# Kernel tuning notes

Measured on AMD Instinct MI355X. Metric: run time of the kernel, lower is better.

The kernel has to match this reference:

```python
import jax, jax.numpy as jnp
import numpy as np

B, T, HID = 2, 2048, 1536
H, HKV, D = 12, 2, 128
EPS = 1e-6
NEG = -1e9


def setup_inputs() -> dict:
    key = jax.random.key(0)
    ks = jax.random.split(key, 8)
    # rotary embeddings built from real angles (cos/sin of position*inv_freq)
    inv_freq = 1.0 / (10000.0 ** (jnp.arange(0, D, 2, dtype=jnp.float32) / D))  # [D/2]
    pos = jnp.arange(T, dtype=jnp.float32)
    ang = pos[:, None] * inv_freq[None, :]                       # [T, D/2]
    emb = jnp.concatenate([ang, ang], axis=-1)                   # [T, D]
    cos = jnp.broadcast_to(jnp.cos(emb)[None], (B, T, D))
    sin = jnp.broadcast_to(jnp.sin(emb)[None], (B, T, D))
    # additive causal mask [1,1,T,T]
    causal = jnp.tril(jnp.ones((T, T), dtype=bool))
    attention_mask = jnp.where(causal, 0.0, NEG).astype(jnp.float32)[None, None]
    s = 0.02
    return {
        "hidden_states": jax.random.normal(ks[0], (B, T, HID), jnp.float32),
        "cos": cos,
        "sin": sin,
        "attention_mask": attention_mask,
        "q_w": jax.random.normal(ks[1], (H * D, HID), jnp.float32) * s,
        "k_w": jax.random.normal(ks[2], (HKV * D, HID), jnp.float32) * s,
        "v_w": jax.random.normal(ks[3], (HKV * D, HID), jnp.float32) * s,
        "o_w": jax.random.normal(ks[4], (HID, H * D), jnp.float32) * s,
        "q_norm_w": jnp.ones((D,), jnp.float32),
        "k_norm_w": jnp.ones((D,), jnp.float32),
    }


def _rms_norm(x, w):
    # per-head RMSNorm over last dim (head_dim), computed in fp32
    xf = x.astype(jnp.float32)
    var = jnp.mean(xf * xf, axis=-1, keepdims=True)
    return (w * (xf * jax.lax.rsqrt(var + EPS))).astype(x.dtype)


def _rotate_half(x):
    x1, x2 = jnp.split(x, 2, axis=-1)
    return jnp.concatenate([-x2, x1], axis=-1)


def reference(hidden_states, cos, sin, attention_mask, q_w, k_w, v_w, o_w, q_norm_w, k_norm_w):
    b, t, _ = hidden_states.shape
    n_rep = H // HKV
    scale = D ** -0.5

    # projections -> [B, n_heads, T, D]
    q = (hidden_states @ q_w.T).reshape(b, t, H, D)
    k = (hidden_states @ k_w.T).reshape(b, t, HKV, D)
    v = (hidden_states @ v_w.T).reshape(b, t, HKV, D).transpose(0, 2, 1, 3)

    # per-head QK RMSNorm, then to [B, H, T, D]
    q = _rms_norm(q, q_norm_w).transpose(0, 2, 1, 3)
    k = _rms_norm(k, k_norm_w).transpose(0, 2, 1, 3)

    # RoPE (cos/sin broadcast over head axis)
    c = cos[:, None, :, :]
    s = sin[:, None, :, :]
    q = q * c + _rotate_half(q) * s
    k = k * c + _rotate_half(k) * s

    # GQA repeat_kv: [B, HKV, T, D] -> [B, H, T, D]
    k = jnp.repeat(k, n_rep, axis=1)
    v = jnp.repeat(v, n_rep, axis=1)

    attn = jnp.einsum('bhqd,bhkd->bhqk', q, k) * scale + attention_mask
    attn = jax.nn.softmax(attn.astype(jnp.float32), axis=-1).astype(q.dtype)
    out = jnp.einsum('bhqk,bhkd->bhqd', attn, v)
    out = out.transpose(0, 2, 1, 3).reshape(b, t, H * D)
    return out @ o_w.T
```

## Files before the change

### kernel.cpp

```cpp
#include <hip/hip_runtime.h>
#include <hip/hip_bf16.h>


#define B_   2
#define T_   2048
#define HID_ 1536
#define H_   12
#define HKV_ 2
#define D_   128
#define GQ_  (H_ / HKV_)
#define NQKV_ 2048
#define SCALE_ 0.08838834764831845f

typedef unsigned short u16;
typedef __attribute__((ext_vector_type(4))) float f32x4;
typedef __attribute__((ext_vector_type(8))) short bf16x8;
typedef __attribute__((ext_vector_type(4))) unsigned short u16x4;
typedef __attribute__((ext_vector_type(8))) unsigned short u16x8;

__device__ __forceinline__ u16 f2b(float f) {
  union { __hip_bfloat16 h; u16 u; } cv;
  cv.h = __float2bfloat16(f);
  return cv.u;
}
__device__ __forceinline__ float b2f(u16 u) {
  union { float f; unsigned i; } cv;
  cv.i = ((unsigned)u) << 16;
  return cv.f;
}

__device__ __forceinline__ void glds16(const u16* g, u16* l) {
  __builtin_amdgcn_global_load_lds((const __attribute__((address_space(1))) void*)g,
                                   (__attribute__((address_space(3))) void*)l, 16, 0, 0);
}

__global__ __launch_bounds__(256) void cvt_f32_bf16(const float* __restrict__ src,
                                                    u16* __restrict__ dst, int n4) {
  int i = blockIdx.x * 256 + threadIdx.x;
  const int stride = gridDim.x * 256;
  for (; i < n4; i += stride) {
    const float4 v = reinterpret_cast<const float4*>(src)[i];
    u16x4 o = {f2b(v.x), f2b(v.y), f2b(v.z), f2b(v.w)};
    reinterpret_cast<u16x4*>(dst)[i] = o;
  }
}

#define NQ4_ 589824
#define NK4_ 98304
__global__ __launch_bounds__(256) void cvt_wqkv(const float* __restrict__ q_w,
                                                const float* __restrict__ k_w,
                                                const float* __restrict__ v_w,
                                                u16* __restrict__ qkvw) {
  int i = blockIdx.x * 256 + threadIdx.x;
  const int stride = gridDim.x * 256;
  const int total = NQ4_ + 2 * NK4_;
  for (; i < total; i += stride) {
    float4 v;
    if (i < NQ4_) v = reinterpret_cast<const float4*>(q_w)[i];
    else if (i < NQ4_ + NK4_) v = reinterpret_cast<const float4*>(k_w)[i - NQ4_];
    else v = reinterpret_cast<const float4*>(v_w)[i - NQ4_ - NK4_];
    u16x4 o = {f2b(v.x), f2b(v.y), f2b(v.z), f2b(v.w)};
    reinterpret_cast<u16x4*>(qkvw)[i] = o;
  }
}

__global__ __launch_bounds__(256) void gemm_bt(const u16* __restrict__ A,
                                               const u16* __restrict__ W,
                                               float* __restrict__ C,
                                               int M, int N, int K) {
  __shared__ __align__(16) u16 As[128 * 64];
  __shared__ __align__(16) u16 Ws[128 * 64];
  const int tid  = threadIdx.x;
  const int lane = tid & 63;
  const int wid  = tid >> 6;
  const int wr = wid >> 1, wc = wid & 1;
  const int l15 = lane & 15, kg = lane >> 4;
  const int rowBase = blockIdx.y * 128;
  const int colBase = blockIdx.x * 128;

  const int srow = lane >> 3;
  const int scol = (lane & 7) << 3;
  const u16* Ab = A + (size_t)(rowBase + wid * 32 + srow) * K + scol;
  const u16* Wb = W + (size_t)(colBase + wid * 32 + srow) * K + scol;

  const f32x4 zero4 = {0.f, 0.f, 0.f, 0.f};
  f32x4 acc[4][4];
#pragma unroll
  for (int m = 0; m < 4; ++m)
#pragma unroll
    for (int n = 0; n < 4; ++n) acc[m][n] = zero4;

  for (int k0 = 0; k0 < K; k0 += 64) {
    __syncthreads();
#pragma unroll
    for (int c = 0; c < 4; ++c) {
      glds16(Ab + (size_t)(c * 8) * K + k0, &As[(wid * 4 + c) * 512]);
      glds16(Wb + (size_t)(c * 8) * K + k0, &Ws[(wid * 4 + c) * 512]);
    }
    __syncthreads();
    bf16x8 a[4][2], b[4][2];
#pragma unroll
    for (int m = 0; m < 4; ++m)
#pragma unroll
      for (int ks = 0; ks < 2; ++ks)
        a[m][ks] = *reinterpret_cast<const bf16x8*>(
            &As[(wr * 64 + m * 16 + l15) * 64 + ks * 32 + kg * 8]);
#pragma unroll
    for (int n = 0; n < 4; ++n)
#pragma unroll
      for (int ks = 0; ks < 2; ++ks)
        b[n][ks] = *reinterpret_cast<const bf16x8*>(
            &Ws[(wc * 64 + n * 16 + l15) * 64 + ks * 32 + kg * 8]);
#pragma unroll
    for (int m = 0; m < 4; ++m)
#pragma unroll
      for (int n = 0; n < 4; ++n)
#pragma unroll
        for (int ks = 0; ks < 2; ++ks)
          acc[m][n] = __builtin_amdgcn_mfma_f32_16x16x32_bf16(a[m][ks], b[n][ks],
                                                              acc[m][n], 0, 0, 0);
  }
#pragma unroll
  for (int m = 0; m < 4; ++m) {
    const int row0 = rowBase + wr * 64 + m * 16 + kg * 4;
#pragma unroll
    for (int n = 0; n < 4; ++n) {
      const int col = colBase + wc * 64 + n * 16 + l15;
#pragma unroll
      for (int r = 0; r < 4; ++r) C[(size_t)(row0 + r) * N + col] = acc[m][n][r];
    }
  }
}

__global__ __launch_bounds__(256) void gemm_qkv(
    const u16* __restrict__ A, const u16* __restrict__ W,
    const float* __restrict__ cosb, const float* __restrict__ sinb,
    const float* __restrict__ q_nw, const float* __restrict__ k_nw,
    u16* __restrict__ q_b, u16* __restrict__ k_b, u16* __restrict__ vt_b) {
  __shared__ __align__(16) u16 smem[128 * 137];
  u16* As = smem;
  u16* Ws = smem + 8192;
  const int tid  = threadIdx.x;
  const int lane = tid & 63;
  const int wid  = tid >> 6;
  const int wr = wid >> 1, wc = wid & 1;
  const int l15 = lane & 15, kg = lane >> 4;
  const int rowBase = blockIdx.y * 128;
  const int colBase = blockIdx.x * 128;
  const int K = HID_;

  const int srow = lane >> 3;
  const int scol = (lane & 7) << 3;
  const u16* Ab = A + (size_t)(rowBase + wid * 32 + srow) * K + scol;
  const u16* Wb = W + (size_t)(colBase + wid * 32 + srow) * K + scol;

  const f32x4 zero4 = {0.f, 0.f, 0.f, 0.f};
  f32x4 acc[4][4];
#pragma unroll
  for (int m = 0; m < 4; ++m)
#pragma unroll
    for (int n = 0; n < 4; ++n) acc[m][n] = zero4;

  for (int k0 = 0; k0 < K; k0 += 64) {
    __syncthreads();
#pragma unroll
    for (int c = 0; c < 4; ++c) {
      glds16(Ab + (size_t)(c * 8) * K + k0, &As[(wid * 4 + c) * 512]);
      glds16(Wb + (size_t)(c * 8) * K + k0, &Ws[(wid * 4 + c) * 512]);
    }
    __syncthreads();
    bf16x8 a[4][2], b[4][2];
#pragma unroll
    for (int m = 0; m < 4; ++m)
#pragma unroll
      for (int ks = 0; ks < 2; ++ks)
        a[m][ks] = *reinterpret_cast<const bf16x8*>(
            &As[(wr * 64 + m * 16 + l15) * 64 + ks * 32 + kg * 8]);
#pragma unroll
    for (int n = 0; n < 4; ++n)
#pragma unroll
      for (int ks = 0; ks < 2; ++ks)
        b[n][ks] = *reinterpret_cast<const bf16x8*>(
            &Ws[(wc * 64 + n * 16 + l15) * 64 + ks * 32 + kg * 8]);
#pragma unroll
    for (int m = 0; m < 4; ++m)
#pragma unroll
      for (int n = 0; n < 4; ++n)
#pragma unroll
        for (int ks = 0; ks < 2; ++ks)
          acc[m][n] = __builtin_amdgcn_mfma_f32_16x16x32_bf16(a[m][ks], b[n][ks],
                                                              acc[m][n], 0, 0, 0);
  }

  __syncthreads();
#pragma unroll
  for (int m = 0; m < 4; ++m)
#pragma unroll
    for (int n = 0; n < 4; ++n)
#pragma unroll
      for (int r = 0; r < 4; ++r)
        smem[(wr * 64 + m * 16 + kg * 4 + r) * 137 + wc * 64 + n * 16 + l15] =
            f2b(acc[m][n][r]);
  __syncthreads();

  const int ct = blockIdx.x;
  const int b = rowBase >> 11;
  if (ct < 14) {
    const float* nw = (ct < 12) ? q_nw : k_nw;
    const float nwl = nw[lane], nwh = nw[lane + 64];
    const float sc = (ct < 12) ? SCALE_ : 1.0f;
    u16* dstbase = (ct < 12) ? (q_b + (size_t)(b * H_ + ct) * T_ * D_)
                             : (k_b + (size_t)(b * HKV_ + (ct - 12)) * T_ * D_);
    for (int i = 0; i < 32; ++i) {
      const int row = wid * 32 + i;
      const int tok = rowBase + row;
      const int t = tok & (T_ - 1);
      const float x1 = b2f(smem[row * 137 + lane]);
      const float x2 = b2f(smem[row * 137 + lane + 64]);
      float ss = x1 * x1 + x2 * x2;
#pragma unroll
      for (int msk = 32; msk >= 1; msk >>= 1) ss += __shfl_xor(ss, msk);
      const float rinv = rsqrtf(ss * (1.0f / D_) + 1e-6f);
      const float c1 = cosb[(size_t)tok * D_ + lane];
      const float c2 = cosb[(size_t)tok * D_ + lane + 64];
      const float s1 = sinb[(size_t)tok * D_ + lane];
      const float s2 = sinb[(size_t)tok * D_ + lane + 64];
      const float n1 = x1 * rinv * nwl, n2 = x2 * rinv * nwh;
      u16* dst = dstbase + (size_t)t * D_;
      dst[lane] = f2b((n1 * c1 - n2 * s1) * sc);
      dst[lane + 64] = f2b((n2 * c2 + n1 * s2) * sc);
    }
  } else {
    const int hv = ct - 14;
    const int tp = (lane & 32) | (((lane >> 2) & 3) << 3) | (((lane >> 4) & 1) << 2) |
                   (lane & 3);
    u16* vb = vt_b + (size_t)(b * HKV_ + hv) * D_ * T_;
    const int tb = rowBase & (T_ - 1);
    for (int it = 0; it < 64; ++it) {
      const int d = wid * 32 + (it >> 1), half = it & 1;
      const float x = b2f(smem[(half * 64 + lane) * 137 + d]);
      vb[(size_t)d * T_ + tb + half * 64 + tp] = f2b(x);
    }
  }
}

__constant__ int QT_ARR[40] = {15,15,15,15,14,14,11,11,11,10, 7, 7, 3,
                               14,14,13,13,13,13,12,12,10,10, 9, 9, 6, 6,
                               12,12, 9, 8, 8, 8, 5, 5, 2,
                                4, 4, 1, 0};
__constant__ int C_ARR[40]  = { 0, 1, 2, 3, 0, 1, 0, 1, 2, 0, 0, 1,-1,
                                2, 3, 0, 1, 2, 3, 0, 1, 1, 2, 0, 1, 0, 1,
                                2, 3, 2, 0, 1, 2, 0, 1,-1,
                                0, 1,-1,-1};
__device__ __forceinline__ int nc_of(int qt) { return (qt < 8) ? 2 : ((qt < 12) ? 3 : 4); }
__device__ __forceinline__ int mlbase_of(int qt) {
  return (qt < 8) ? 2 * (qt - 4) : ((qt < 12) ? 8 + 3 * (qt - 8) : 20 + 4 * (qt - 12));
}
__device__ __forceinline__ int pbase_of(int qt) {
  return (qt < 8) ? (qt - 4) : ((qt < 12) ? 4 + 2 * (qt - 8) : 12 + 3 * (qt - 12));
}

__global__ __launch_bounds__(256) void attn_kernel(const u16* __restrict__ q_b,
                                                   const u16* __restrict__ k_b,
                                                   const u16* __restrict__ vt_b,
                                                   u16* __restrict__ aout,
                                                   u16* __restrict__ po0,
                                                   float2* __restrict__ ml) {
  __shared__ __align__(16) u16 Ks[2][64 * 128];
  __shared__ __align__(16) u16 Vs[2][128 * 64];
  const int id = blockIdx.x;
  const int item = id / 24;
  const int bh = id - item * 24;
  const int qt = QT_ARR[item];
  const int c = C_ARR[item];
  int kt0, ktend;
  bool partial;
  if (c < 0) {
    kt0 = 0; ktend = 2 * qt + 1; partial = false;
  } else {
    const int nt = 2 * qt + 2;
    const int nc = nc_of(qt);
    const int base = nt / nc, rem = nt - base * nc;
    kt0 = c * base + (c < rem ? c : rem);
    ktend = kt0 + base + (c < rem ? 1 : 0) - 1;
    partial = true;
  }
  const int b = bh / H_, h = bh - b * H_;
  const int kvh = h / GQ_;
  const int tid = threadIdx.x;
  const int w = tid >> 6, lane = tid & 63;
  const int l15 = lane & 15, kg = lane >> 4;
  const int qbase = qt * 128;

  const u16* Kb = k_b + (size_t)(b * HKV_ + kvh) * T_ * D_;
  const u16* Vb = vt_b + (size_t)(b * HKV_ + kvh) * D_ * T_;

  bf16x8 qf[2][4];
#pragma unroll
  for (int qb = 0; qb < 2; ++qb) {
    const u16* qrow =
        q_b + ((size_t)(b * H_ + h) * T_ + qbase + w * 32 + qb * 16 + l15) * D_;
#pragma unroll
    for (int s4 = 0; s4 < 4; ++s4)
      qf[qb][s4] = *reinterpret_cast<const bf16x8*>(qrow + s4 * 32 + kg * 8);
  }

  int kK[4], vK[4];
#pragma unroll
  for (int cc = 0; cc < 4; ++cc) {
    const int ch = w * 4 + cc;
    const int kr = ch * 4 + (lane >> 4);
    kK[cc] = kr * D_ + (((lane & 15) << 3) ^ ((kr & 7) << 3));
    const int dr = ch * 8 + (lane >> 3);
    vK[cc] = dr * T_ + (((lane & 7) << 3) ^ ((dr & 7) << 3));
  }
  const int xorv = (l15 & 7) << 3;

  const f32x4 zero4 = {0.f, 0.f, 0.f, 0.f};
  f32x4 o[2][8];
#pragma unroll
  for (int qb = 0; qb < 2; ++qb)
#pragma unroll
    for (int n = 0; n < 8; ++n) o[qb][n] = zero4;
  float m[2] = {0.f, 0.f};
  float lsum[2] = {0.f, 0.f};

  {
    const size_t kb = (size_t)kt0 * 64;
#pragma unroll
    for (int cc = 0; cc < 4; ++cc) {
      glds16(Kb + kb * D_ + kK[cc], &Ks[0][(w * 4 + cc) * 512]);
      glds16(Vb + kb + vK[cc], &Vs[0][(w * 4 + cc) * 512]);
    }
  }
  int cur = 0;

  for (int kt = kt0; kt <= ktend; ++kt) {
    if (kt < ktend) {
      const size_t kb = (size_t)(kt + 1) * 64;
#pragma unroll
      for (int cc = 0; cc < 4; ++cc) {
        glds16(Kb + kb * D_ + kK[cc], &Ks[cur ^ 1][(w * 4 + cc) * 512]);
        glds16(Vb + kb + vK[cc], &Vs[cur ^ 1][(w * 4 + cc) * 512]);
      }
      asm volatile("s_waitcnt vmcnt(8)" ::: "memory");
    } else {
      asm volatile("s_waitcnt vmcnt(0)" ::: "memory");
    }
    __builtin_amdgcn_s_barrier();
    asm volatile("" ::: "memory");

    const u16* Kc = &Ks[cur][0];
    const u16* Vc = &Vs[cur][0];
    f32x4 sc[2][4];
#pragma unroll
    for (int qb = 0; qb < 2; ++qb)
#pragma unroll
      for (int n = 0; n < 4; ++n) sc[qb][n] = zero4;
    __builtin_amdgcn_s_setprio(1);
#pragma unroll
    for (int n = 0; n < 4; ++n)
#pragma unroll
      for (int s4 = 0; s4 < 4; ++s4) {
        const int koff = (n * 16 + l15) * 128 + ((s4 * 32 + kg * 8) ^ xorv);
        bf16x8 kf = *reinterpret_cast<const bf16x8*>(&Kc[koff]);
#pragma unroll
        for (int qb = 0; qb < 2; ++qb)
          sc[qb][n] = __builtin_amdgcn_mfma_f32_16x16x32_bf16(kf, qf[qb][s4],
                                                              sc[qb][n], 0, 0, 0);
      }
    __builtin_amdgcn_s_setprio(0);
    if (kt >= 2 * qt) {
#pragma unroll
      for (int qb = 0; qb < 2; ++qb) {
        const int qg = w * 32 + qb * 16 + l15;
        const int kbb = (kt - 2 * qt) * 64;
#pragma unroll
        for (int n = 0; n < 4; ++n)
#pragma unroll
          for (int r = 0; r < 4; ++r)
            if (kbb + n * 16 + kg * 4 + r > qg) sc[qb][n][r] = -3e38f;
      }
    }
    float pm[2];
#pragma unroll
    for (int qb = 0; qb < 2; ++qb) {
      float v = sc[qb][0][0];
#pragma unroll
      for (int n = 0; n < 4; ++n)
#pragma unroll
        for (int r = 0; r < 4; ++r) v = fmaxf(v, sc[qb][n][r]);
      v = fmaxf(v, __shfl_xor(v, 16));
      v = fmaxf(v, __shfl_xor(v, 32));
      pm[qb] = v;
    }
    if (__any((pm[0] > m[0] + 8.f) | (pm[1] > m[1] + 8.f))) {
#pragma unroll
      for (int qb = 0; qb < 2; ++qb) {
        const float mn = fmaxf(m[qb], pm[qb]);
        const float al = __expf(m[qb] - mn);
        m[qb] = mn;
        lsum[qb] *= al;
        float alT[4];
#pragma unroll
        for (int r = 0; r < 4; ++r)
          alT[r] = __shfl(al, (lane & 48) | (kg * 4 + r));
#pragma unroll
        for (int n = 0; n < 8; ++n)
#pragma unroll
          for (int r = 0; r < 4; ++r) o[qb][n][r] *= alT[r];
      }
    }
#pragma unroll
    for (int qb = 0; qb < 2; ++qb) {
      float rs = 0.f;
#pragma unroll
      for (int n = 0; n < 4; ++n)
#pragma unroll
        for (int r = 0; r < 4; ++r) {
          const float p = __expf(sc[qb][n][r] - m[qb]);
          sc[qb][n][r] = p;
          rs += p;
        }
      rs += __shfl_xor(rs, 16);
      rs += __shfl_xor(rs, 32);
      lsum[qb] += rs;
    }
    bf16x8 pf[2][2];
#pragma unroll
    for (int qb = 0; qb < 2; ++qb)
#pragma unroll
      for (int ks = 0; ks < 2; ++ks)
#pragma unroll
        for (int r = 0; r < 4; ++r) {
          pf[qb][ks][r] = (short)f2b(sc[qb][2 * ks][r]);
          pf[qb][ks][r + 4] = (short)f2b(sc[qb][2 * ks + 1][r]);
        }
    __builtin_amdgcn_s_setprio(1);
#pragma unroll
    for (int n = 0; n < 8; ++n)
#pragma unroll
      for (int ks = 0; ks < 2; ++ks) {
        const int voff = (n * 16 + l15) * 64 + ((ks * 32 + kg * 8) ^ xorv);
        bf16x8 vf = *reinterpret_cast<const bf16x8*>(&Vc[voff]);
#pragma unroll
        for (int qb = 0; qb < 2; ++qb)
          o[qb][n] = __builtin_amdgcn_mfma_f32_16x16x32_bf16(pf[qb][ks], vf,
                                                             o[qb][n], 0, 0, 0);
      }
    __builtin_amdgcn_s_setprio(0);
    __builtin_amdgcn_s_barrier();
    cur ^= 1;
  }

  if (!partial) {
    float invT[2][4];
#pragma unroll
    for (int qb = 0; qb < 2; ++qb) {
      const float inv = 1.0f / lsum[qb];
#pragma unroll
      for (int r = 0; r < 4; ++r)
        invT[qb][r] = __shfl(inv, (lane & 48) | (kg * 4 + r));
    }
#pragma unroll
    for (int qb = 0; qb < 2; ++qb) {
      const int t0 = qbase + w * 32 + qb * 16 + kg * 4;
#pragma unroll
      for (int n = 0; n < 8; ++n)
#pragma unroll
        for (int r = 0; r < 4; ++r)
          aout[(size_t)(b * T_ + t0 + r) * (H_ * D_) + h * D_ + n * 16 + l15] =
              f2b(o[qb][n][r] * invT[qb][r]);
    }
  } else {
    const int mlslot = bh * 36 + mlbase_of(qt) + c;
    if (kg == 0) {
#pragma unroll
      for (int qb = 0; qb < 2; ++qb) {
        float2 v;
        v.x = m[qb];
        v.y = lsum[qb];
        ml[(size_t)mlslot * 128 + w * 32 + qb * 16 + l15] = v;
      }
    }
    if (c == 0) {
#pragma unroll
      for (int qb = 0; qb < 2; ++qb) {
        const int t0 = qbase + w * 32 + qb * 16 + kg * 4;
#pragma unroll
        for (int n = 0; n < 8; ++n)
#pragma unroll
          for (int r = 0; r < 4; ++r)
            aout[(size_t)(b * T_ + t0 + r) * (H_ * D_) + h * D_ + n * 16 + l15] =
                f2b(o[qb][n][r]);
      }
    } else {
      const int pslot = bh * 24 + pbase_of(qt) + (c - 1);
#pragma unroll
      for (int qb = 0; qb < 2; ++qb) {
        const int row0 = w * 32 + qb * 16 + kg * 4;
#pragma unroll
        for (int n = 0; n < 8; ++n)
#pragma unroll
          for (int r = 0; r < 4; ++r)
            po0[((size_t)pslot * 128 + row0 + r) * 128 + n * 16 + l15] =
                f2b(o[qb][n][r]);
      }
    }
  }
}

__global__ __launch_bounds__(256) void combine_kernel(u16* __restrict__ aout,
                                                      const u16* __restrict__ po0,
                                                      const float2* __restrict__ ml) {
  const int qt = 4 + blockIdx.x;
  const int bh = blockIdx.y;
  const int nc = nc_of(qt);
  const int mlb = bh * 36 + mlbase_of(qt);
  const int pb = bh * 24 + pbase_of(qt);
  const int b = bh / H_, h = bh - b * H_;
  const int t0 = qt * 128;
  const int tid = threadIdx.x;
  const int row = tid >> 1;
  const int colc = (tid & 1) << 6;

  float ms[4], ls[4];
  float mm = -3e38f;
  for (int cc = 0; cc < nc; ++cc) {
    const float2 v = ml[(size_t)(mlb + cc) * 128 + row];
    ms[cc] = v.x; ls[cc] = v.y;
    mm = fmaxf(mm, v.x);
  }
  float lt = 0.f;
  float scl[4];
  for (int cc = 0; cc < nc; ++cc) {
    scl[cc] = __expf(ms[cc] - mm);
    lt += ls[cc] * scl[cc];
  }
  const float inv = 1.0f / lt;
  for (int cc = 0; cc < nc; ++cc) scl[cc] *= inv;

  u16* a = aout + (size_t)(b * T_ + t0 + row) * (H_ * D_) + h * D_ + colc;
#pragma unroll
  for (int j = 0; j < 8; ++j) {
    u16x8 v0 = *reinterpret_cast<const u16x8*>(a + j * 8);
    float acc[8];
#pragma unroll
    for (int e = 0; e < 8; ++e) acc[e] = b2f(v0[e]) * scl[0];
    for (int cc = 1; cc < nc; ++cc) {
      const u16* p = po0 + ((size_t)(pb + cc - 1) * 128 + row) * 128 + colc;
      u16x8 vc = *reinterpret_cast<const u16x8*>(p + j * 8);
#pragma unroll
      for (int e = 0; e < 8; ++e) acc[e] += b2f(vc[e]) * scl[cc];
    }
    u16x8 outv;
#pragma unroll
    for (int e = 0; e < 8; ++e) outv[e] = f2b(acc[e]);
    *reinterpret_cast<u16x8*>(a + j * 8) = outv;
  }
}

extern "C" void kernel_launch(void* const* d_in, const int* in_sizes, int n_in,
                              void* d_out, int out_size, void* d_ws, size_t ws_size,
                              hipStream_t stream) {
  const float* hidden = (const float*)d_in[0];
  const float* cosb   = (const float*)d_in[1];
  const float* sinb   = (const float*)d_in[2];
  const float* q_w  = (const float*)d_in[4];
  const float* k_w  = (const float*)d_in[5];
  const float* v_w  = (const float*)d_in[6];
  const float* o_w  = (const float*)d_in[7];
  const float* q_nw = (const float*)d_in[8];
  const float* k_nw = (const float*)d_in[9];
  float* out = (float*)d_out;

  char* ws = (char*)d_ws;
  const size_t MB = 1u << 20;
  u16*    hidden_b = (u16*)(ws);
  u16*    qkvw     = (u16*)(ws + 12 * MB);
  u16*    q_b      = (u16*)(ws + 18 * MB);
  u16*    k_b      = (u16*)(ws + 30 * MB);
  u16*    vt_b     = (u16*)(ws + 32 * MB);
  u16*    aout     = (u16*)(ws);
  u16*    owb      = (u16*)(ws + 12 * MB);
  float2* ml       = (float2*)(ws + 17 * MB);
  u16*    po0      = (u16*)d_out;

  const dim3 blk(256);
  const int M = B_ * T_;

  cvt_f32_bf16<<<2048, blk, 0, stream>>>(hidden, hidden_b, (B_ * T_ * HID_) / 4);
  cvt_wqkv<<<3072, blk, 0, stream>>>(q_w, k_w, v_w, qkvw);

  gemm_qkv<<<dim3(NQKV_ / 128, M / 128), blk, 0, stream>>>(
      hidden_b, qkvw, cosb, sinb, q_nw, k_nw, q_b, k_b, vt_b);

  cvt_f32_bf16<<<2048, blk, 0, stream>>>(o_w, owb, (H_ * D_ * HID_) / 4);

  attn_kernel<<<960, blk, 0, stream>>>(q_b, k_b, vt_b, aout, po0, ml);
  combine_kernel<<<dim3(12, B_ * H_), blk, 0, stream>>>(aout, po0, ml);

  gemm_bt<<<dim3(HID_ / 128, M / 128), blk, 0, stream>>>(aout, owb, out,
                                                         M, HID_, HID_);
}
```

Measured before the change: 202.1 us.

## Double-buffer LDS in both GEMMs and fuse input conversion kernels

Both GEMM kernels now use two LDS buffers, issuing the global-to-LDS loads for the next K tile before running the MFMAs on the current one. This cuts the per-iteration barriers from two to one and raises wave priority around the MFMA block. The hidden-state and QKV-weight fp32-to-bf16 conversions are merged into one launch to save a kernel dispatch. Doubling shared memory per block may lower occupancy, and the single waitcnt(0) barrier still serialises at every tile.

Result: faster. 189.8 us (-6.1%).

```diff
diff --git a/kernel.cpp b/kernel.cpp
--- a/kernel.cpp
+++ b/kernel.cpp
@@ -45,22 +45,33 @@
   }
 }
 
+#define NH4_ 1572864
 #define NQ4_ 589824
 #define NK4_ 98304
-__global__ __launch_bounds__(256) void cvt_wqkv(const float* __restrict__ q_w,
-                                                const float* __restrict__ k_w,
-                                                const float* __restrict__ v_w,
-                                                u16* __restrict__ qkvw) {
+__global__ __launch_bounds__(256) void cvt_inputs(const float* __restrict__ hidden,
+                                                  const float* __restrict__ q_w,
+                                                  const float* __restrict__ k_w,
+                                                  const float* __restrict__ v_w,
+                                                  u16* __restrict__ hidden_b,
+                                                  u16* __restrict__ qkvw) {
   int i = blockIdx.x * 256 + threadIdx.x;
   const int stride = gridDim.x * 256;
-  const int total = NQ4_ + 2 * NK4_;
+  const int total = NH4_ + NQ4_ + 2 * NK4_;
   for (; i < total; i += stride) {
     float4 v;
-    if (i < NQ4_) v = reinterpret_cast<const float4*>(q_w)[i];
-    else if (i < NQ4_ + NK4_) v = reinterpret_cast<const float4*>(k_w)[i - NQ4_];
-    else v = reinterpret_cast<const float4*>(v_w)[i - NQ4_ - NK4_];
+    u16x4* dst;
+    if (i < NH4_) {
+      v = reinterpret_cast<const float4*>(hidden)[i];
+      dst = reinterpret_cast<u16x4*>(hidden_b) + i;
+    } else {
+      const int j = i - NH4_;
+      if (j < NQ4_) v = reinterpret_cast<const float4*>(q_w)[j];
+      else if (j < NQ4_ + NK4_) v = reinterpret_cast<const float4*>(k_w)[j - NQ4_];
+      else v = reinterpret_cast<const float4*>(v_w)[j - NQ4_ - NK4_];
+      dst = reinterpret_cast<u16x4*>(qkvw) + j;
+    }
     u16x4 o = {f2b(v.x), f2b(v.y), f2b(v.z), f2b(v.w)};
-    reinterpret_cast<u16x4*>(qkvw)[i] = o;
+    *dst = o;
   }
 }
 
@@ -68,8 +79,8 @@
                                                const u16* __restrict__ W,
                                                float* __restrict__ C,
                                                int M, int N, int K) {
-  __shared__ __align__(16) u16 As[128 * 64];
-  __shared__ __align__(16) u16 Ws[128 * 64];
+  __shared__ __align__(16) u16 As[2][128 * 64];
+  __shared__ __align__(16) u16 Ws[2][128 * 64];
   const int tid  = threadIdx.x;
   const int lane = tid & 63;
   const int wid  = tid >> 6;
@@ -90,27 +101,40 @@
 #pragma unroll
     for (int n = 0; n < 4; ++n) acc[m][n] = zero4;
 
-  for (int k0 = 0; k0 < K; k0 += 64) {
-    __syncthreads();
-#pragma unroll
-    for (int c = 0; c < 4; ++c) {
-      glds16(Ab + (size_t)(c * 8) * K + k0, &As[(wid * 4 + c) * 512]);
-      glds16(Wb + (size_t)(c * 8) * K + k0, &Ws[(wid * 4 + c) * 512]);
-    }
-    __syncthreads();
+  const int nt = K >> 6;
+#pragma unroll
+  for (int c = 0; c < 4; ++c) {
+    glds16(Ab + (size_t)(c * 8) * K, &As[0][(wid * 4 + c) * 512]);
+    glds16(Wb + (size_t)(c * 8) * K, &Ws[0][(wid * 4 + c) * 512]);
+  }
+  asm volatile("s_waitcnt vmcnt(0)" ::: "memory");
+  __builtin_amdgcn_s_barrier();
+  asm volatile("" ::: "memory");
+  int cur = 0;
+
+  for (int t = 0; t < nt; ++t) {
+    if (t + 1 < nt) {
+      const int k0 = (t + 1) << 6;
+#pragma unroll
+      for (int c = 0; c < 4; ++c) {
+        glds16(Ab + (size_t)(c * 8) * K + k0, &As[cur ^ 1][(wid * 4 + c) * 512]);
+        glds16(Wb + (size_t)(c * 8) * K + k0, &Ws[cur ^ 1][(wid * 4 + c) * 512]);
+      }
+    }
     bf16x8 a[4][2], b[4][2];
 #pragma unroll
     for (int m = 0; m < 4; ++m)
 #pragma unroll
       for (int ks = 0; ks < 2; ++ks)
         a[m][ks] = *reinterpret_cast<const bf16x8*>(
-            &As[(wr * 64 + m * 16 + l15) * 64 + ks * 32 + kg * 8]);
+            &As[cur][(wr * 64 + m * 16 + l15) * 64 + ks * 32 + kg * 8]);
 #pragma unroll
     for (int n = 0; n < 4; ++n)
 #pragma unroll
       for (int ks = 0; ks < 2; ++ks)
         b[n][ks] = *reinterpret_cast<const bf16x8*>(
-            &Ws[(wc * 64 + n * 16 + l15) * 64 + ks * 32 + kg * 8]);
+            &Ws[cur][(wc * 64 + n * 16 + l15) * 64 + ks * 32 + kg * 8]);
+    __builtin_amdgcn_s_setprio(1);
 #pragma unroll
     for (int m = 0; m < 4; ++m)
 #pragma unroll
@@ -119,6 +143,13 @@
         for (int ks = 0; ks < 2; ++ks)
           acc[m][n] = __builtin_amdgcn_mfma_f32_16x16x32_bf16(a[m][ks], b[n][ks],
                                                               acc[m][n], 0, 0, 0);
+    __builtin_amdgcn_s_setprio(0);
+    if (t + 1 < nt) {
+      asm volatile("s_waitcnt vmcnt(0)" ::: "memory");
+      __builtin_amdgcn_s_barrier();
+      asm volatile("" ::: "memory");
+      cur ^= 1;
+    }
   }
 #pragma unroll
   for (int m = 0; m < 4; ++m) {
@@ -137,9 +168,7 @@
     const float* __restrict__ cosb, const float* __restrict__ sinb,
     const float* __restrict__ q_nw, const float* __restrict__ k_nw,
     u16* __restrict__ q_b, u16* __restrict__ k_b, u16* __restrict__ vt_b) {
-  __shared__ __align__(16) u16 smem[128 * 137];
-  u16* As = smem;
-  u16* Ws = smem + 8192;
+  __shared__ __align__(16) u16 smem[32768];
   const int tid  = threadIdx.x;
   const int lane = tid & 63;
   const int wid  = tid >> 6;
@@ -161,27 +190,42 @@
 #pragma unroll
     for (int n = 0; n < 4; ++n) acc[m][n] = zero4;
 
-  for (int k0 = 0; k0 < K; k0 += 64) {
-    __syncthreads();
-#pragma unroll
-    for (int c = 0; c < 4; ++c) {
-      glds16(Ab + (size_t)(c * 8) * K + k0, &As[(wid * 4 + c) * 512]);
-      glds16(Wb + (size_t)(c * 8) * K + k0, &Ws[(wid * 4 + c) * 512]);
-    }
-    __syncthreads();
+  const int nt = K >> 6;
+#pragma unroll
+  for (int c = 0; c < 4; ++c) {
+    glds16(Ab + (size_t)(c * 8) * K, &smem[(wid * 4 + c) * 512]);
+    glds16(Wb + (size_t)(c * 8) * K, &smem[8192 + (wid * 4 + c) * 512]);
+  }
+  asm volatile("s_waitcnt vmcnt(0)" ::: "memory");
+  __builtin_amdgcn_s_barrier();
+  asm volatile("" ::: "memory");
+  int cur = 0;
+
+  for (int t = 0; t < nt; ++t) {
+    if (t + 1 < nt) {
+      const int k0 = (t + 1) << 6;
+      const int ob = (cur ^ 1) * 16384;
+#pragma unroll
+      for (int c = 0; c < 4; ++c) {
+        glds16(Ab + (size_t)(c * 8) * K + k0, &smem[ob + (wid * 4 + c) * 512]);
+        glds16(Wb + (size_t)(c * 8) * K + k0, &smem[ob + 8192 + (wid * 4 + c) * 512]);
+      }
+    }
+    const int ib = cur * 16384;
     bf16x8 a[4][2], b[4][2];
 #pragma unroll
     for (int m = 0; m < 4; ++m)
 #pragma unroll
       for (int ks = 0; ks < 2; ++ks)
         a[m][ks] = *reinterpret_cast<const bf16x8*>(
-            &As[(wr * 64 + m * 16 + l15) * 64 + ks * 32 + kg * 8]);
+            &smem[ib + (wr * 64 + m * 16 + l15) * 64 + ks * 32 + kg * 8]);
 #pragma unroll
     for (int n = 0; n < 4; ++n)
 #pragma unroll
       for (int ks = 0; ks < 2; ++ks)
         b[n][ks] = *reinterpret_cast<const bf16x8*>(
-            &Ws[(wc * 64 + n * 16 + l15) * 64 + ks * 32 + kg * 8]);
+            &smem[ib + 8192 + (wc * 64 + n * 16 + l15) * 64 + ks * 32 + kg * 8]);
+    __builtin_amdgcn_s_setprio(1);
 #pragma unroll
     for (int m = 0; m < 4; ++m)
 #pragma unroll
@@ -190,6 +234,13 @@
         for (int ks = 0; ks < 2; ++ks)
           acc[m][n] = __builtin_amdgcn_mfma_f32_16x16x32_bf16(a[m][ks], b[n][ks],
                                                               acc[m][n], 0, 0, 0);
+    __builtin_amdgcn_s_setprio(0);
+    if (t + 1 < nt) {
+      asm volatile("s_waitcnt vmcnt(0)" ::: "memory");
+      __builtin_amdgcn_s_barrier();
+      asm volatile("" ::: "memory");
+      cur ^= 1;
+    }
   }
 
   __syncthreads();
@@ -589,8 +640,7 @@
   const dim3 blk(256);
   const int M = B_ * T_;
 
-  cvt_f32_bf16<<<2048, blk, 0, stream>>>(hidden, hidden_b, (B_ * T_ * HID_) / 4);
-  cvt_wqkv<<<3072, blk, 0, stream>>>(q_w, k_w, v_w, qkvw);
+  cvt_inputs<<<2048, blk, 0, stream>>>(hidden, q_w, k_w, v_w, hidden_b, qkvw);
 
   gemm_qkv<<<dim3(NQKV_ / 128, M / 128), blk, 0, stream>>>(
       hidden_b, qkvw, cosb, sinb, q_nw, k_nw, q_b, k_b, vt_b);
```
